# Kernel tuning notes

Hardware: AMD Instinct MI355X
Metric: run time of the kernel (lower is better)

Reference implementation:

```python
import jax, jax.numpy as jnp
import numpy as np

N_NODES = 50000
N_EDGES = 500000
NODE_IN = 128
EDGE_IN = 64
HID = 128
OUT = 1


def _linear_params(key, fan_in, fan_out):
    # torch nn.Linear default init: U(-1/sqrt(fan_in), 1/sqrt(fan_in))
    kw, kb = jax.random.split(key)
    bound = 1.0 / np.sqrt(fan_in)
    W = jax.random.uniform(kw, (fan_in, fan_out), jnp.float32, -bound, bound)
    b = jax.random.uniform(kb, (fan_out,), jnp.float32, -bound, bound)
    return W, b


def setup_inputs() -> dict:
    key = jax.random.key(0)
    ks = jax.random.split(key, 8)
    x = jax.random.normal(ks[0], (N_NODES, NODE_IN), jnp.float32)
    edge_index = jax.random.randint(ks[1], (2, N_EDGES), 0, N_NODES, jnp.int64)
    edge_attr = jax.random.normal(ks[2], (N_EDGES, EDGE_IN), jnp.float32)
    Wn, bn = _linear_params(ks[3], NODE_IN, HID)
    We, be = _linear_params(ks[4], EDGE_IN, HID)
    W1, b1 = _linear_params(ks[5], HID * 3, HID * 4)
    W2, b2 = _linear_params(ks[6], HID * 4, HID * 2)
    W3, b3 = _linear_params(ks[7], HID * 2, OUT)
    return {
        "x": x, "edge_index": edge_index, "edge_attr": edge_attr,
        "Wn": Wn, "bn": bn, "We": We, "be": be,
        "W1": W1, "b1": b1, "W2": W2, "b2": b2, "W3": W3, "b3": b3,
    }


def reference(x, edge_index, edge_attr, Wn, bn, We, be, W1, b1, W2, b2, W3, b3):
    src, dst = edge_index[0], edge_index[1]
    node_f = jax.nn.relu(x @ Wn + bn)          # [N, H]
    edge_f = jax.nn.relu(edge_attr @ We + be)  # [E, H]
    combined = jnp.concatenate([node_f[src], node_f[dst], edge_f], axis=1)  # [E, 3H]
    h = jax.nn.relu(combined @ W1 + b1)        # [E, 4H]
    h = jax.nn.relu(h @ W2 + b2)               # [E, 2H]
    return h @ W3 + b3                          # [E, OUT]
```

## Files before the change

kernel.cpp:

```cpp
#include <hip/hip_runtime.h>
#include <hip/hip_bf16.h>
#include <stdint.h>

#define N_NODES 50000
#define N_EDGES 500000
#define NODE_IN 128
#define EDGE_IN 64
#define HID 128
#define K_H1 384
#define N_H1 512
#define N_H2 256

#define EPB 64

typedef short s8v __attribute__((ext_vector_type(8)));
typedef float f4v __attribute__((ext_vector_type(4)));

__device__ __forceinline__ unsigned int pk_bf16(float a, float b) {
    union { __hip_bfloat162 h; unsigned int u; } c;
    c.h = __float22bfloat162_rn(float2{a, b});
    return c.u;
}

__device__ __forceinline__ s8v load_a_f32(const float* __restrict__ base, int row, int ld, int koff) {
    const float4* p = (const float4*)(base + row * ld + koff);
    float4 x0 = p[0];
    float4 x1 = p[1];
    union { s8v v; unsigned int u[4]; } r;
    r.u[0] = pk_bf16(x0.x, x0.y);
    r.u[1] = pk_bf16(x0.z, x0.w);
    r.u[2] = pk_bf16(x1.x, x1.y);
    r.u[3] = pk_bf16(x1.z, x1.w);
    return r.v;
}

__device__ __forceinline__ void pack_one(const float* __restrict__ src, unsigned short* __restrict__ dst,
                                         int idx, int N) {
    int j = idx & 7;
    int lane = (idx >> 3) & 63;
    int rest = idx >> 9;
    int NT = N >> 4;
    int nt = rest % NT;
    int kb = rest / NT;
    int n = nt * 16 + (lane & 15);
    int k = kb * 32 + ((lane >> 4) << 3) + j;
    union { __hip_bfloat16 h; unsigned short s; } c;
    c.h = __float2bfloat16(src[k * N + n]);
    dst[idx] = c.s;
}

#define WN_ELEMS (NODE_IN * HID)
#define WE_ELEMS (EDGE_IN * HID)
#define W1_ELEMS (K_H1 * N_H1)
#define W2_ELEMS (N_H1 * N_H2)
#define PACK_TOTAL (WN_ELEMS + WE_ELEMS + W1_ELEMS + W2_ELEMS)

__global__ void pack_all(const float* __restrict__ Wn, const float* __restrict__ We,
                         const float* __restrict__ W1, const float* __restrict__ W2,
                         unsigned short* __restrict__ Wnp, unsigned short* __restrict__ Wep,
                         unsigned short* __restrict__ W1p, unsigned short* __restrict__ W2p) {
    int idx = blockIdx.x * blockDim.x + threadIdx.x;
    if (idx >= PACK_TOTAL) return;
    if (idx < WN_ELEMS) { pack_one(Wn, Wnp, idx, HID); return; }
    idx -= WN_ELEMS;
    if (idx < WE_ELEMS) { pack_one(We, Wep, idx, HID); return; }
    idx -= WE_ELEMS;
    if (idx < W1_ELEMS) { pack_one(W1, W1p, idx, N_H1); return; }
    idx -= W1_ELEMS;
    pack_one(W2, W2p, idx, N_H2);
}

__global__ __launch_bounds__(256, 4) void node_feat_kernel(
    const float* __restrict__ x, const unsigned short* __restrict__ Wnp,
    const float* __restrict__ bn, unsigned short* __restrict__ node_f)
{
    int tid = threadIdx.x;
    int wave = tid >> 6, lane = tid & 63;
    int lm = lane & 15, quad = lane >> 4;
    int row0 = blockIdx.x * 64;
    int node = row0 + wave * 16 + lm;
    int nodec = node < N_NODES ? node : N_NODES - 1;

    f4v zero = {0.f, 0.f, 0.f, 0.f};
    f4v acc[8];
    #pragma unroll
    for (int mt = 0; mt < 8; ++mt) acc[mt] = zero;

    for (int kb = 0; kb < 4; ++kb) {
        s8v b = load_a_f32(x, nodec, NODE_IN, kb * 32 + quad * 8);
        #pragma unroll
        for (int mt = 0; mt < 8; ++mt) {
            s8v a = *(const s8v*)(Wnp + (((kb * 8 + mt) * 64 + lane) << 3));
            acc[mt] = __builtin_amdgcn_mfma_f32_16x16x32_bf16(a, b, acc[mt], 0, 0, 0);
        }
    }

    if (node < N_NODES) {
        #pragma unroll
        for (int mt = 0; mt < 8; ++mt) {
            float4 bv = *(const float4*)(bn + mt * 16 + quad * 4);
            uint2 pk;
            pk.x = pk_bf16(fmaxf(acc[mt][0] + bv.x, 0.f), fmaxf(acc[mt][1] + bv.y, 0.f));
            pk.y = pk_bf16(fmaxf(acc[mt][2] + bv.z, 0.f), fmaxf(acc[mt][3] + bv.w, 0.f));
            *(uint2*)(node_f + node * HID + mt * 16 + quad * 4) = pk;
        }
    }
}

#define CSTR 392
#define H1STR 520

__global__ __launch_bounds__(512, 4) void fused_edge_kernel(
    const int* __restrict__ edge_index, const float* __restrict__ edge_attr,
    const unsigned short* __restrict__ node_f,
    const unsigned short* __restrict__ Wep, const float* __restrict__ be,
    const unsigned short* __restrict__ W1p, const float* __restrict__ b1,
    const unsigned short* __restrict__ W2p, const float* __restrict__ b2,
    const float* __restrict__ W3, const float* __restrict__ b3,
    float* __restrict__ out)
{
    __shared__ __align__(16) unsigned short smem[EPB * H1STR];
    __shared__ float out_lds[EPB];

    int tid = threadIdx.x;
    int wave = tid >> 6, lane = tid & 63;
    int lm = lane & 15, quad = lane >> 4;
    int e0 = blockIdx.x * EPB;

    if (tid < EPB) out_lds[tid] = 0.f;

    int gi = tid >> 3, gp = tid & 7;
    uint4 gs0, gs1, gd0, gd1;
    {
        int e = e0 + gi;
        int ec = e < N_EDGES ? e : N_EDGES - 1;
        int s = edge_index[ec];
        int d = edge_index[N_EDGES + ec];
        const uint4* ps = (const uint4*)(node_f + s * HID + gp * 16);
        const uint4* pd = (const uint4*)(node_f + d * HID + gp * 16);
        gs0 = ps[0]; gs1 = ps[1];
        gd0 = pd[0]; gd1 = pd[1];
    }

    {
        int nt = wave & 3;
        int mbase = (wave >> 2) * 4;
        int erow = e0 + nt * 16 + lm;
        if (erow >= N_EDGES) erow = N_EDGES - 1;

        f4v zero = {0.f, 0.f, 0.f, 0.f};
        f4v acc[4];
        #pragma unroll
        for (int t = 0; t < 4; ++t) acc[t] = zero;

        for (int kb = 0; kb < 2; ++kb) {
            s8v b = load_a_f32(edge_attr, erow, EDGE_IN, kb * 32 + quad * 8);
            #pragma unroll
            for (int t = 0; t < 4; ++t) {
                s8v a = *(const s8v*)(Wep + (((kb * 8 + mbase + t) * 64 + lane) << 3));
                acc[t] = __builtin_amdgcn_mfma_f32_16x16x32_bf16(a, b, acc[t], 0, 0, 0);
            }
        }
        {
            uint4* cs = (uint4*)(smem + gi * CSTR + gp * 16);
            uint4* cd = (uint4*)(smem + gi * CSTR + 128 + gp * 16);
            cs[0] = gs0; cs[1] = gs1;
            cd[0] = gd0; cd[1] = gd1;
        }
        int edge = nt * 16 + lm;
        #pragma unroll
        for (int t = 0; t < 4; ++t) {
            int col = (mbase + t) * 16 + quad * 4;
            float4 bv = *(const float4*)(be + col);
            uint2 pk;
            pk.x = pk_bf16(fmaxf(acc[t][0] + bv.x, 0.f), fmaxf(acc[t][1] + bv.y, 0.f));
            pk.y = pk_bf16(fmaxf(acc[t][2] + bv.z, 0.f), fmaxf(acc[t][3] + bv.w, 0.f));
            *(uint2*)(smem + edge * CSTR + 256 + col) = pk;
        }
    }
    __syncthreads();

    f4v zero = {0.f, 0.f, 0.f, 0.f};
    f4v acc1[4][4];
    #pragma unroll
    for (int t = 0; t < 4; ++t)
        #pragma unroll
        for (int nt = 0; nt < 4; ++nt) acc1[t][nt] = zero;

    {
        s8v afr[4];
        #pragma unroll
        for (int t = 0; t < 4; ++t)
            afr[t] = *(const s8v*)(W1p + (((0 * 32 + wave * 4 + t) * 64 + lane) << 3));
        for (int kb = 0; kb < 12; ++kb) {
            s8v bfr[4];
            #pragma unroll
            for (int nt = 0; nt < 4; ++nt)
                bfr[nt] = *(const s8v*)(smem + (nt * 16 + lm) * CSTR + kb * 32 + quad * 8);
            int kbn = kb < 11 ? kb + 1 : 11;
            s8v anx[4];
            #pragma unroll
            for (int t = 0; t < 4; ++t)
                anx[t] = *(const s8v*)(W1p + (((kbn * 32 + wave * 4 + t) * 64 + lane) << 3));
            #pragma unroll
            for (int t = 0; t < 4; ++t)
                #pragma unroll
                for (int nt = 0; nt < 4; ++nt)
                    acc1[t][nt] = __builtin_amdgcn_mfma_f32_16x16x32_bf16(afr[t], bfr[nt], acc1[t][nt], 0, 0, 0);
            #pragma unroll
            for (int t = 0; t < 4; ++t) afr[t] = anx[t];
        }
    }
    __syncthreads();

    #pragma unroll
    for (int t = 0; t < 4; ++t) {
        int col = (wave * 4 + t) * 16 + quad * 4;
        float4 bv = *(const float4*)(b1 + col);
        #pragma unroll
        for (int nt = 0; nt < 4; ++nt) {
            int edge = nt * 16 + lm;
            uint2 pk;
            pk.x = pk_bf16(fmaxf(acc1[t][nt][0] + bv.x, 0.f), fmaxf(acc1[t][nt][1] + bv.y, 0.f));
            pk.y = pk_bf16(fmaxf(acc1[t][nt][2] + bv.z, 0.f), fmaxf(acc1[t][nt][3] + bv.w, 0.f));
            *(uint2*)(smem + edge * H1STR + col) = pk;
        }
    }
    __syncthreads();

    f4v acc2[2][4];
    #pragma unroll
    for (int t = 0; t < 2; ++t)
        #pragma unroll
        for (int nt = 0; nt < 4; ++nt) acc2[t][nt] = zero;

    {
        s8v afr[2];
        #pragma unroll
        for (int t = 0; t < 2; ++t)
            afr[t] = *(const s8v*)(W2p + (((0 * 16 + wave * 2 + t) * 64 + lane) << 3));
        for (int kb = 0; kb < 16; ++kb) {
            s8v bfr[4];
            #pragma unroll
            for (int nt = 0; nt < 4; ++nt)
                bfr[nt] = *(const s8v*)(smem + (nt * 16 + lm) * H1STR + kb * 32 + quad * 8);
            int kbn = kb < 15 ? kb + 1 : 15;
            s8v anx[2];
            #pragma unroll
            for (int t = 0; t < 2; ++t)
                anx[t] = *(const s8v*)(W2p + (((kbn * 16 + wave * 2 + t) * 64 + lane) << 3));
            #pragma unroll
            for (int t = 0; t < 2; ++t)
                #pragma unroll
                for (int nt = 0; nt < 4; ++nt)
                    acc2[t][nt] = __builtin_amdgcn_mfma_f32_16x16x32_bf16(afr[t], bfr[nt], acc2[t][nt], 0, 0, 0);
            #pragma unroll
            for (int t = 0; t < 2; ++t) afr[t] = anx[t];
        }
    }

    {
        float4 b2v[2], w3v[2];
        #pragma unroll
        for (int t = 0; t < 2; ++t) {
            int col = (wave * 2 + t) * 16 + quad * 4;
            b2v[t] = *(const float4*)(b2 + col);
            w3v[t] = *(const float4*)(W3 + col);
        }
        #pragma unroll
        for (int nt = 0; nt < 4; ++nt) {
            float p = 0.f;
            #pragma unroll
            for (int t = 0; t < 2; ++t) {
                p += fmaxf(acc2[t][nt][0] + b2v[t].x, 0.f) * w3v[t].x;
                p += fmaxf(acc2[t][nt][1] + b2v[t].y, 0.f) * w3v[t].y;
                p += fmaxf(acc2[t][nt][2] + b2v[t].z, 0.f) * w3v[t].z;
                p += fmaxf(acc2[t][nt][3] + b2v[t].w, 0.f) * w3v[t].w;
            }
            p += __shfl_xor(p, 16);
            p += __shfl_xor(p, 32);
            if (quad == 0)
                atomicAdd(&out_lds[nt * 16 + lm], p);
        }
    }
    __syncthreads();

    if (tid < EPB) {
        int e = e0 + tid;
        if (e < N_EDGES) out[e] = out_lds[tid] + b3[0];
    }
}

extern "C" void kernel_launch(void* const* d_in, const int* in_sizes, int n_in,
                              void* d_out, int out_size, void* d_ws, size_t ws_size,
                              hipStream_t stream)
{
    const float* x          = (const float*)d_in[0];
    const int*   edge_index = (const int*)d_in[1];
    const float* edge_attr  = (const float*)d_in[2];
    const float* Wn = (const float*)d_in[3];
    const float* bn = (const float*)d_in[4];
    const float* We = (const float*)d_in[5];
    const float* be = (const float*)d_in[6];
    const float* W1 = (const float*)d_in[7];
    const float* b1 = (const float*)d_in[8];
    const float* W2 = (const float*)d_in[9];
    const float* b2 = (const float*)d_in[10];
    const float* W3 = (const float*)d_in[11];
    const float* b3 = (const float*)d_in[12];
    float* out = (float*)d_out;

    char* ws = (char*)d_ws;
    unsigned short* node_f = (unsigned short*)ws;
    unsigned short* Wnp = (unsigned short*)(ws + 12800000);
    unsigned short* Wep = (unsigned short*)(ws + 12832768);
    unsigned short* W1p = (unsigned short*)(ws + 12849152);
    unsigned short* W2p = (unsigned short*)(ws + 13242368);

    pack_all<<<(PACK_TOTAL + 255) / 256, 256, 0, stream>>>(Wn, We, W1, W2, Wnp, Wep, W1p, W2p);

    node_feat_kernel<<<(N_NODES + 63) / 64, 256, 0, stream>>>(x, Wnp, bn, node_f);

    fused_edge_kernel<<<(N_EDGES + EPB - 1) / EPB, 512, 0, stream>>>(
        edge_index, edge_attr, node_f, Wep, be, W1p, b1, W2p, b2, W3, b3, out);
}
```

Before: 581.1 us.

## Double edge tile per block to halve weight-fragment reloads in fused MLP

Raises the edges per block from 64 to 128, so each wave computes 8 edge n-tiles against its W1/W2 fragments. Each weight fragment fetched from global memory now feeds twice as many MFMAs. The W2 loop also prefetches the next k-step's LDS B fragments into registers, and the W1 loop drops the clamp on its next-step weight index. The workspace is reordered so that the final over-read of W1p lands inside W2p. In exchange the LDS tile doubles, which likely allows only one block per CU, and register pressure rises with the larger accumulator arrays.

```diff
diff --git a/kernel.cpp b/kernel.cpp
--- a/kernel.cpp
+++ b/kernel.cpp
@@ -11,7 +11,7 @@
 #define N_H1 512
 #define N_H2 256
 
-#define EPB 64
+#define EPB 128
 
 typedef short s8v __attribute__((ext_vector_type(8)));
 typedef float f4v __attribute__((ext_vector_type(4)));
@@ -110,7 +110,7 @@
 #define CSTR 392
 #define H1STR 520
 
-__global__ __launch_bounds__(512, 4) void fused_edge_kernel(
+__global__ __launch_bounds__(512, 2) void fused_edge_kernel(
     const int* __restrict__ edge_index, const float* __restrict__ edge_attr,
     const unsigned short* __restrict__ node_f,
     const unsigned short* __restrict__ Wep, const float* __restrict__ be,
@@ -129,48 +129,46 @@
 
     if (tid < EPB) out_lds[tid] = 0.f;
 
-    int gi = tid >> 3, gp = tid & 7;
-    uint4 gs0, gs1, gd0, gd1;
+    int gi = tid >> 2, gp = tid & 3;
+    uint4 gs[4], gd[4];
     {
         int e = e0 + gi;
         int ec = e < N_EDGES ? e : N_EDGES - 1;
         int s = edge_index[ec];
         int d = edge_index[N_EDGES + ec];
-        const uint4* ps = (const uint4*)(node_f + s * HID + gp * 16);
-        const uint4* pd = (const uint4*)(node_f + d * HID + gp * 16);
-        gs0 = ps[0]; gs1 = ps[1];
-        gd0 = pd[0]; gd1 = pd[1];
-    }
-
-    {
-        int nt = wave & 3;
-        int mbase = (wave >> 2) * 4;
-        int erow = e0 + nt * 16 + lm;
+        const uint4* ps = (const uint4*)(node_f + s * HID + gp * 32);
+        const uint4* pd = (const uint4*)(node_f + d * HID + gp * 32);
+        #pragma unroll
+        for (int c = 0; c < 4; ++c) { gs[c] = ps[c]; gd[c] = pd[c]; }
+    }
+
+    {
+        int erow = e0 + wave * 16 + lm;
         if (erow >= N_EDGES) erow = N_EDGES - 1;
 
         f4v zero = {0.f, 0.f, 0.f, 0.f};
-        f4v acc[4];
-        #pragma unroll
-        for (int t = 0; t < 4; ++t) acc[t] = zero;
+        f4v acc[8];
+        #pragma unroll
+        for (int t = 0; t < 8; ++t) acc[t] = zero;
 
         for (int kb = 0; kb < 2; ++kb) {
             s8v b = load_a_f32(edge_attr, erow, EDGE_IN, kb * 32 + quad * 8);
             #pragma unroll
-            for (int t = 0; t < 4; ++t) {
-                s8v a = *(const s8v*)(Wep + (((kb * 8 + mbase + t) * 64 + lane) << 3));
+            for (int t = 0; t < 8; ++t) {
+                s8v a = *(const s8v*)(Wep + (((kb * 8 + t) * 64 + lane) << 3));
                 acc[t] = __builtin_amdgcn_mfma_f32_16x16x32_bf16(a, b, acc[t], 0, 0, 0);
             }
         }
         {
-            uint4* cs = (uint4*)(smem + gi * CSTR + gp * 16);
-            uint4* cd = (uint4*)(smem + gi * CSTR + 128 + gp * 16);
-            cs[0] = gs0; cs[1] = gs1;
-            cd[0] = gd0; cd[1] = gd1;
-        }
-        int edge = nt * 16 + lm;
-        #pragma unroll
-        for (int t = 0; t < 4; ++t) {
-            int col = (mbase + t) * 16 + quad * 4;
+            uint4* cs = (uint4*)(smem + gi * CSTR + gp * 32);
+            uint4* cd = (uint4*)(smem + gi * CSTR + 128 + gp * 32);
+            #pragma unroll
+            for (int c = 0; c < 4; ++c) { cs[c] = gs[c]; cd[c] = gd[c]; }
+        }
+        int edge = wave * 16 + lm;
+        #pragma unroll
+        for (int t = 0; t < 8; ++t) {
+            int col = t * 16 + quad * 4;
             float4 bv = *(const float4*)(be + col);
             uint2 pk;
             pk.x = pk_bf16(fmaxf(acc[t][0] + bv.x, 0.f), fmaxf(acc[t][1] + bv.y, 0.f));
@@ -181,31 +179,38 @@
     __syncthreads();
 
     f4v zero = {0.f, 0.f, 0.f, 0.f};
-    f4v acc1[4][4];
+    f4v acc1[4][8];
     #pragma unroll
     for (int t = 0; t < 4; ++t)
         #pragma unroll
-        for (int nt = 0; nt < 4; ++nt) acc1[t][nt] = zero;
-
-    {
+        for (int nt = 0; nt < 8; ++nt) acc1[t][nt] = zero;
+
+    {
+        const unsigned short* bb0 = smem + lm * CSTR + quad * 8;
+        const unsigned short* bb4 = bb0 + 4 * 16 * CSTR;
+        const unsigned short* wb = W1p + (((wave * 4) * 64 + lane) << 3);
+
         s8v afr[4];
         #pragma unroll
-        for (int t = 0; t < 4; ++t)
-            afr[t] = *(const s8v*)(W1p + (((0 * 32 + wave * 4 + t) * 64 + lane) << 3));
+        for (int t = 0; t < 4; ++t) afr[t] = *(const s8v*)(wb + t * 512);
+
+        #pragma unroll 1
         for (int kb = 0; kb < 12; ++kb) {
-            s8v bfr[4];
+            s8v bfr[8];
             #pragma unroll
             for (int nt = 0; nt < 4; ++nt)
-                bfr[nt] = *(const s8v*)(smem + (nt * 16 + lm) * CSTR + kb * 32 + quad * 8);
-            int kbn = kb < 11 ? kb + 1 : 11;
+                bfr[nt] = *(const s8v*)(bb0 + kb * 32 + nt * (16 * CSTR));
+            #pragma unroll
+            for (int nt = 0; nt < 4; ++nt)
+                bfr[nt + 4] = *(const s8v*)(bb4 + kb * 32 + nt * (16 * CSTR));
             s8v anx[4];
             #pragma unroll
             for (int t = 0; t < 4; ++t)
-                anx[t] = *(const s8v*)(W1p + (((kbn * 32 + wave * 4 + t) * 64 + lane) << 3));
+                anx[t] = *(const s8v*)(wb + (kb + 1) * (32 * 64 * 8) + t * 512);
             #pragma unroll
             for (int t = 0; t < 4; ++t)
                 #pragma unroll
-                for (int nt = 0; nt < 4; ++nt)
+                for (int nt = 0; nt < 8; ++nt)
                     acc1[t][nt] = __builtin_amdgcn_mfma_f32_16x16x32_bf16(afr[t], bfr[nt], acc1[t][nt], 0, 0, 0);
             #pragma unroll
             for (int t = 0; t < 4; ++t) afr[t] = anx[t];
@@ -218,7 +223,7 @@
         int col = (wave * 4 + t) * 16 + quad * 4;
         float4 bv = *(const float4*)(b1 + col);
         #pragma unroll
-        for (int nt = 0; nt < 4; ++nt) {
+        for (int nt = 0; nt < 8; ++nt) {
             int edge = nt * 16 + lm;
             uint2 pk;
             pk.x = pk_bf16(fmaxf(acc1[t][nt][0] + bv.x, 0.f), fmaxf(acc1[t][nt][1] + bv.y, 0.f));
@@ -228,32 +233,45 @@
     }
     __syncthreads();
 
-    f4v acc2[2][4];
+    f4v acc2[2][8];
     #pragma unroll
     for (int t = 0; t < 2; ++t)
         #pragma unroll
-        for (int nt = 0; nt < 4; ++nt) acc2[t][nt] = zero;
-
-    {
-        s8v afr[2];
-        #pragma unroll
-        for (int t = 0; t < 2; ++t)
-            afr[t] = *(const s8v*)(W2p + (((0 * 16 + wave * 2 + t) * 64 + lane) << 3));
+        for (int nt = 0; nt < 8; ++nt) acc2[t][nt] = zero;
+
+    {
+        const unsigned short* hb0 = smem + lm * H1STR + quad * 8;
+        const unsigned short* hb4 = hb0 + 4 * 16 * H1STR;
+        const unsigned short* wb = W2p + (((wave * 2) * 64 + lane) << 3);
+
+        s8v bfr[8], afr[2];
+        #pragma unroll
+        for (int nt = 0; nt < 4; ++nt) {
+            bfr[nt]     = *(const s8v*)(hb0 + nt * (16 * H1STR));
+            bfr[nt + 4] = *(const s8v*)(hb4 + nt * (16 * H1STR));
+        }
+        #pragma unroll
+        for (int t = 0; t < 2; ++t) afr[t] = *(const s8v*)(wb + t * 512);
+
+        #pragma unroll 1
         for (int kb = 0; kb < 16; ++kb) {
-            s8v bfr[4];
-            #pragma unroll
-            for (int nt = 0; nt < 4; ++nt)
-                bfr[nt] = *(const s8v*)(smem + (nt * 16 + lm) * H1STR + kb * 32 + quad * 8);
             int kbn = kb < 15 ? kb + 1 : 15;
-            s8v anx[2];
+            s8v bnx[8], anx[2];
+            #pragma unroll
+            for (int nt = 0; nt < 4; ++nt) {
+                bnx[nt]     = *(const s8v*)(hb0 + kbn * 32 + nt * (16 * H1STR));
+                bnx[nt + 4] = *(const s8v*)(hb4 + kbn * 32 + nt * (16 * H1STR));
+            }
             #pragma unroll
             for (int t = 0; t < 2; ++t)
-                anx[t] = *(const s8v*)(W2p + (((kbn * 16 + wave * 2 + t) * 64 + lane) << 3));
+                anx[t] = *(const s8v*)(wb + kbn * (16 * 64 * 8) + t * 512);
             #pragma unroll
             for (int t = 0; t < 2; ++t)
                 #pragma unroll
-                for (int nt = 0; nt < 4; ++nt)
+                for (int nt = 0; nt < 8; ++nt)
                     acc2[t][nt] = __builtin_amdgcn_mfma_f32_16x16x32_bf16(afr[t], bfr[nt], acc2[t][nt], 0, 0, 0);
+            #pragma unroll
+            for (int nt = 0; nt < 8; ++nt) bfr[nt] = bnx[nt];
             #pragma unroll
             for (int t = 0; t < 2; ++t) afr[t] = anx[t];
         }
@@ -268,7 +286,7 @@
             w3v[t] = *(const float4*)(W3 + col);
         }
         #pragma unroll
-        for (int nt = 0; nt < 4; ++nt) {
+        for (int nt = 0; nt < 8; ++nt) {
             float p = 0.f;
             #pragma unroll
             for (int t = 0; t < 2; ++t) {
@@ -312,10 +330,10 @@
 
     char* ws = (char*)d_ws;
     unsigned short* node_f = (unsigned short*)ws;
-    unsigned short* Wnp = (unsigned short*)(ws + 12800000);
-    unsigned short* Wep = (unsigned short*)(ws + 12832768);
-    unsigned short* W1p = (unsigned short*)(ws + 12849152);
-    unsigned short* W2p = (unsigned short*)(ws + 13242368);
+    unsigned short* W1p = (unsigned short*)(ws + 12800000);
+    unsigned short* W2p = (unsigned short*)(ws + 13193216);
+    unsigned short* Wnp = (unsigned short*)(ws + 13455360);
+    unsigned short* Wep = (unsigned short*)(ws + 13488128);
 
     pack_all<<<(PACK_TOTAL + 255) / 256, 256, 0, stream>>>(Wn, We, W1, W2, Wnp, Wep, W1p, W2p);
 
```

Result: no change. 574.8 us (-1.1%).
